# Kernel optimization log

Measured on AMD Instinct MI355X. Metric: run time of the kernel, lower is better.

## Reference

```python
import jax, jax.numpy as jnp
import numpy as np

N = 100000
NFEAT = 128
NHID = 128
NCLASS = 40
E = 1600000
EPS = 1e-5


def _spmm(vals, src, dst, x, n):
    # y[dst] += vals * x[src]  (sparse adj @ x)
    return jax.ops.segment_sum(vals[:, None] * x[src], dst, num_segments=n)


def _bn(h, gamma, beta, rmean, rvar):
    # BatchNorm1d in eval mode (running statistics)
    return (h - rmean) * jax.lax.rsqrt(rvar + EPS) * gamma + beta


def setup_inputs() -> dict:
    key = jax.random.key(0)
    ks = jax.random.split(key, 24)
    inp = {
        'x': jax.random.normal(ks[0], (N, NFEAT), dtype=jnp.float32),
        'M': jax.random.uniform(ks[1], (N, 1), dtype=jnp.float32),
        'AM': jax.random.uniform(ks[2], (N, 1), dtype=jnp.float32),
        'srcZ': jax.random.randint(ks[3], (E,), 0, N, dtype=jnp.int32),
        'dstZ': jax.random.randint(ks[4], (E,), 0, N, dtype=jnp.int32),
        'valsZ': jax.random.uniform(ks[5], (E,), dtype=jnp.float32),
        'src': jax.random.randint(ks[6], (E,), 0, N, dtype=jnp.int32),
        'dst': jax.random.randint(ks[7], (E,), 0, N, dtype=jnp.int32),
        'vals': jax.random.uniform(ks[8], (E,), dtype=jnp.float32),
        # layer 0 (PaGConv) params
        'W0': jax.random.normal(ks[9], (NHID, NFEAT), dtype=jnp.float32) * (1.414 / np.sqrt(NFEAT)),
        'b0': jnp.zeros((NHID,), dtype=jnp.float32),
        'g0': jnp.ones((NHID,), dtype=jnp.float32),
        'be0': jnp.zeros((NHID,), dtype=jnp.float32),
        'rm0': jax.random.normal(ks[10], (NHID,), dtype=jnp.float32) * 0.1,
        'rv0': jax.random.uniform(ks[11], (NHID,), dtype=jnp.float32) + 0.5,
        # layer 1 (GConv) params
        'W1': jax.random.normal(ks[12], (NHID, NHID), dtype=jnp.float32) * (1.414 / np.sqrt(NHID)),
        'b1': jnp.zeros((NHID,), dtype=jnp.float32),
        'g1': jnp.ones((NHID,), dtype=jnp.float32),
        'be1': jnp.zeros((NHID,), dtype=jnp.float32),
        'rm1': jax.random.normal(ks[13], (NHID,), dtype=jnp.float32) * 0.1,
        'rv1': jax.random.uniform(ks[14], (NHID,), dtype=jnp.float32) + 0.5,
        # layer 2 (GConv) params
        'W2': jax.random.normal(ks[15], (NCLASS, NHID), dtype=jnp.float32) * (1.414 / np.sqrt(NHID)),
        'b2': jnp.zeros((NCLASS,), dtype=jnp.float32),
    }
    return inp


def reference(x, M, AM, srcZ, dstZ, valsZ, src, dst, vals,
              W0, b0, g0, be0, rm0, rv0,
              W1, b1, g1, be1, rm1, rv1,
              W2, b2):
    n = x.shape[0]
    # layer 0: PaGConv with adjZ: fc(spmm(adjZ, M*x) * AM), then BN + ReLU (dropout off in eval)
    h = _spmm(valsZ, srcZ, dstZ, M * x, n) * AM
    h = h @ W0.T + b0
    h = jax.nn.relu(_bn(h, g0, be0, rm0, rv0))
    # layer 1: GConv with adj: fc(spmm(adj, h)), then BN + ReLU
    h = _spmm(vals, src, dst, h, n)
    h = h @ W1.T + b1
    h = jax.nn.relu(_bn(h, g1, be1, rm1, rv1))
    # layer 2: GConv, then log_softmax
    h = _spmm(vals, src, dst, h, n)
    h = h @ W2.T + b2
    return jax.nn.log_softmax(h, axis=-1)
```

## Files before the change

kernel.cpp:

```cpp
#include <hip/hip_runtime.h>
#include <math.h>

#define NFEAT 128
#define NCLS 40
#define NCLSP 64
#define BINROWS 64
#define NBINMAX 1600
#define NBLKC 256
#define CHUNKMAX 6400
#define SEGC 7
#define RSMAX 2048

typedef short bf16x8 __attribute__((ext_vector_type(8)));
typedef float f32x4 __attribute__((ext_vector_type(4)));

__device__ __forceinline__ float bf2f(unsigned int lo16) {
  return __uint_as_float((lo16 & 0xffffu) << 16);
}
__device__ __forceinline__ unsigned int f2bf(float x) {
  unsigned int u = __float_as_uint(x);
  return (u + 0x7fffu + ((u >> 16) & 1u)) >> 16;
}

__global__ void bn_prep(const float* b0, const float* g0, const float* be0,
                        const float* rm0, const float* rv0,
                        const float* b1, const float* g1, const float* be1,
                        const float* rm1, const float* rv1,
                        float* sc0, float* sh0, float* sc1, float* sh1) {
  int t = threadIdx.x;
  if (t < 128) {
    float s = g0[t] * rsqrtf(rv0[t] + 1e-5f);
    sc0[t] = s;
    sh0[t] = (b0[t] - rm0[t]) * s + be0[t];
  } else {
    int i = t - 128;
    float s = g1[i] * rsqrtf(rv1[i] + 1e-5f);
    sc1[i] = s;
    sh1[i] = (b1[i] - rm1[i]) * s + be1[i];
  }
}

__global__ void convert_xm(const float* __restrict__ x, const float* __restrict__ Mv,
                           unsigned short* __restrict__ xm, int n) {
  int i = blockIdx.x * 256 + threadIdx.x;
  if (i >= n * (NFEAT / 8)) return;
  int row = i >> 4;
  float m = Mv[row];
  const float4* p = (const float4*)(x + (size_t)i * 8);
  float4 v0 = p[0], v1 = p[1];
  unsigned int o0 = f2bf(v0.x * m) | (f2bf(v0.y * m) << 16);
  unsigned int o1 = f2bf(v0.z * m) | (f2bf(v0.w * m) << 16);
  unsigned int o2 = f2bf(v1.x * m) | (f2bf(v1.y * m) << 16);
  unsigned int o3 = f2bf(v1.z * m) | (f2bf(v1.w * m) << 16);
  ((uint4*)xm)[i] = make_uint4(o0, o1, o2, o3);
}

__global__ void convert_w(const float* __restrict__ W0, const float* __restrict__ W1,
                          const float* __restrict__ W2,
                          unsigned short* __restrict__ Wb0, unsigned short* __restrict__ Wb1,
                          unsigned short* __restrict__ W2hi, unsigned short* __restrict__ W2lo) {
  int i = blockIdx.x * 256 + threadIdx.x;
  if (i < 4096) {
    const float* W = (i < 2048) ? W0 : W1;
    unsigned short* Wb = (i < 2048) ? Wb0 : Wb1;
    int j = (i < 2048) ? i : i - 2048;
    const float4* p = (const float4*)(W + (size_t)j * 8);
    float4 v0 = p[0], v1 = p[1];
    unsigned int o0 = f2bf(v0.x) | (f2bf(v0.y) << 16);
    unsigned int o1 = f2bf(v0.z) | (f2bf(v0.w) << 16);
    unsigned int o2 = f2bf(v1.x) | (f2bf(v1.y) << 16);
    unsigned int o3 = f2bf(v1.z) | (f2bf(v1.w) << 16);
    ((uint4*)Wb)[j] = make_uint4(o0, o1, o2, o3);
  } else {
    int j = i - 4096;
    int r = j >> 4;
    float v[8] = {0.f, 0.f, 0.f, 0.f, 0.f, 0.f, 0.f, 0.f};
    if (r < NCLS) {
      const float4* p = (const float4*)(W2 + (size_t)j * 8);
      float4 a = p[0], b = p[1];
      v[0] = a.x; v[1] = a.y; v[2] = a.z; v[3] = a.w;
      v[4] = b.x; v[5] = b.y; v[6] = b.z; v[7] = b.w;
    }
    unsigned int h[8], l[8];
#pragma unroll
    for (int q = 0; q < 8; ++q) {
      h[q] = f2bf(v[q]);
      l[q] = f2bf(v[q] - bf2f(h[q]));
    }
    ((uint4*)W2hi)[j] = make_uint4(h[0] | (h[1] << 16), h[2] | (h[3] << 16),
                                   h[4] | (h[5] << 16), h[6] | (h[7] << 16));
    ((uint4*)W2lo)[j] = make_uint4(l[0] | (l[1] << 16), l[2] | (l[3] << 16),
                                   l[4] | (l[5] << 16), l[6] | (l[7] << 16));
  }
}

__global__ __launch_bounds__(256) void bin_sort1(
    const int* __restrict__ srcp, const int* __restrict__ dstp, const float* __restrict__ valp,
    int2* __restrict__ Drm, int2* __restrict__ binsC, int E, int nbin, int chunk) {
  __shared__ int2 stage[CHUNKMAX];
  __shared__ int cur[NBINMAX];
  __shared__ int ps[256];
  const int t = threadIdx.x, k = blockIdx.x;
  for (int i = t; i < nbin; i += 256) cur[i] = 0;
  __syncthreads();
  const int e0 = k * chunk, e1 = min(E, e0 + chunk);
#pragma unroll 4
  for (int e = e0 + t; e < e1; e += 256) atomicAdd(&cur[dstp[e] >> 6], 1);
  __syncthreads();
  int loc[SEGC], cnt[SEGC];
  int s = 0;
#pragma unroll
  for (int j = 0; j < SEGC; ++j) {
    int i = t * SEGC + j;
    int v = (i < nbin) ? cur[i] : 0;
    loc[j] = s; cnt[j] = v;
    s += v;
  }
  ps[t] = s;
  __syncthreads();
  for (int o = 1; o < 256; o <<= 1) {
    int x = (t >= o) ? ps[t - o] : 0;
    __syncthreads();
    ps[t] += x;
    __syncthreads();
  }
  int ex = ps[t] - s;
#pragma unroll
  for (int j = 0; j < SEGC; ++j) {
    int i = t * SEGC + j;
    if (i < nbin) {
      int o = ex + loc[j];
      Drm[(size_t)k * nbin + i] = make_int2(e0 + o, cnt[j]);
      cur[i] = o;
    }
  }
  __syncthreads();
#pragma unroll 2
  for (int e = e0 + t; e < e1; e += 256) {
    int d = dstp[e];
    int p = atomicAdd(&cur[d >> 6], 1);
    stage[p] = make_int2(srcp[e] | ((d & 63) << 17), __float_as_int(valp[e]));
  }
  __syncthreads();
  const int n = e1 - e0;
  for (int i = t; i < n; i += 256) binsC[e0 + i] = stage[i];
}

__global__ __launch_bounds__(256) void transposeD1(
    const int2* __restrict__ Drm, int2* __restrict__ Dbm, int* __restrict__ binTot, int nbin) {
  __shared__ int2 st[8][256];
  __shared__ int part[256];
  int t = threadIdx.x;
  int i0 = blockIdx.x * 8;
#pragma unroll
  for (int j = 0; j < 8; ++j) {
    int i = i0 + j;
    st[j][t] = (i < nbin) ? Drm[(size_t)t * nbin + i] : make_int2(0, 0);
  }
  __syncthreads();
  {
    int j = t >> 5, ks = (t & 31) * 8;
    int i = i0 + j;
    if (i < nbin) {
      int2* q = &Dbm[(size_t)i * NBLKC + ks];
#pragma unroll
      for (int m = 0; m < 8; ++m) q[m] = st[j][ks + m];
    }
    int p = 0;
#pragma unroll
    for (int m = 0; m < 8; ++m) p += st[j][ks + m].y;
    part[t] = p;
  }
  __syncthreads();
  if (t < 8) {
    int s = 0;
    for (int k = 0; k < 32; ++k) s += part[t * 32 + k];
    if (i0 + t < nbin) binTot[i0 + t] = s;
  }
}

__global__ __launch_bounds__(256) void bin_start1(
    const int* __restrict__ bt, int* __restrict__ bs, int nbin) {
  __shared__ int ps[256];
  int t = threadIdx.x;
  int C = (nbin + 255) / 256;
  int loc[SEGC + 1];
  int sum = 0;
  for (int j = 0; j < C; ++j) {
    int i = t * C + j;
    loc[j] = sum;
    sum += (i < nbin) ? bt[i] : 0;
  }
  ps[t] = sum;
  __syncthreads();
  for (int o = 1; o < 256; o <<= 1) {
    int x = (t >= o) ? ps[t - o] : 0;
    __syncthreads();
    ps[t] += x;
    __syncthreads();
  }
  int ex = ps[t] - sum;
  for (int j = 0; j < C; ++j) {
    int i = t * C + j;
    if (i < nbin) bs[i] = ex + loc[j];
  }
  if (t == 255) bs[nbin] = ps[255];
}

__global__ __launch_bounds__(256) void row_sort(
    const int2* __restrict__ Dbm, const int2* __restrict__ binsC,
    const int* __restrict__ binStart, int2* __restrict__ bins2,
    int* __restrict__ rowptr, int n, int nbin) {
  __shared__ int2 stage[RSMAX];
  __shared__ int ps[256];
  __shared__ int rcnt[BINROWS];
  __shared__ int roff[BINROWS];
  const int b = blockIdx.x, t = threadIdx.x;
  if (t < BINROWS) rcnt[t] = 0;
  int2 run = Dbm[(size_t)b * NBLKC + t];
  ps[t] = run.y;
  __syncthreads();
  for (int o = 1; o < 256; o <<= 1) {
    int x = (t >= o) ? ps[t - o] : 0;
    __syncthreads();
    ps[t] += x;
    __syncthreads();
  }
  int mystart = ps[t] - run.y;
  for (int j = 0; j < run.y; ++j) {
    int2 en = binsC[run.x + j];
    int idx = mystart + j;
    if (idx < RSMAX) stage[idx] = en;
    atomicAdd(&rcnt[(en.x >> 17) & 63], 1);
  }
  __syncthreads();
  const int bs = binStart[b];
  if (t < BINROWS) {
    int c = rcnt[t];
    int s = c;
#pragma unroll
    for (int o = 1; o < 64; o <<= 1) {
      int v = __shfl_up(s, o);
      if (t >= o) s += v;
    }
    int excl = s - c;
    int row = b * BINROWS + t;
    if (row < n) rowptr[row] = bs + excl;
    roff[t] = excl;
  }
  __syncthreads();
  int total = min(ps[255], RSMAX);
  for (int i = t; i < total; i += 256) {
    int2 en = stage[i];
    int row = (en.x >> 17) & 63;
    int p = atomicAdd(&roff[row], 1);
    bins2[bs + p] = en;
  }
  if (b == nbin - 1 && t == 0) rowptr[n] = binStart[nbin];
}

template <bool SCALE>
__global__ __launch_bounds__(256) void spmm128_sorted(
    const int* __restrict__ rowptr, const int2* __restrict__ bins2,
    const unsigned short* __restrict__ X, const float* __restrict__ AM,
    unsigned short* __restrict__ Y, int n) {
  int row = (blockIdx.x * 256 + threadIdx.x) >> 6;
  int lane = threadIdx.x & 63;
  if (row >= n) return;
  int s = rowptr[row], d = rowptr[row + 1] - s;
  int eidx = lane >> 4, l16 = lane & 15;
  float acc[8] = {0.f, 0.f, 0.f, 0.f, 0.f, 0.f, 0.f, 0.f};
  for (int kb = 0; kb < d; kb += 64) {
    int rem = min(64, d - kb);
    int2 my = (lane < rem) ? bins2[s + kb + lane] : make_int2(0, 0);
    int myc = my.x & 0x1FFFF;
    float myw = __int_as_float(my.y);
    int steps = (rem + 3) >> 2;
#pragma unroll 4
    for (int st = 0; st < steps; ++st) {
      int idx = st * 4 + eidx;
      int c = __shfl(myc, idx);
      float wv = __shfl(myw, idx);
      uint4 pv = *(const uint4*)(X + (size_t)c * NFEAT + l16 * 8);
      acc[0] += wv * bf2f(pv.x);
      acc[1] += wv * bf2f(pv.x >> 16);
      acc[2] += wv * bf2f(pv.y);
      acc[3] += wv * bf2f(pv.y >> 16);
      acc[4] += wv * bf2f(pv.z);
      acc[5] += wv * bf2f(pv.z >> 16);
      acc[6] += wv * bf2f(pv.w);
      acc[7] += wv * bf2f(pv.w >> 16);
    }
  }
#pragma unroll
  for (int j = 0; j < 8; ++j) {
    acc[j] += __shfl_xor(acc[j], 16);
    acc[j] += __shfl_xor(acc[j], 32);
  }
  if (SCALE) {
    float am = AM[row];
#pragma unroll
    for (int j = 0; j < 8; ++j) acc[j] *= am;
  }
  if (eidx == 0) {
    uint4 pk;
    pk.x = f2bf(acc[0]) | (f2bf(acc[1]) << 16);
    pk.y = f2bf(acc[2]) | (f2bf(acc[3]) << 16);
    pk.z = f2bf(acc[4]) | (f2bf(acc[5]) << 16);
    pk.w = f2bf(acc[6]) | (f2bf(acc[7]) << 16);
    *(uint4*)(Y + (size_t)row * NFEAT + l16 * 8) = pk;
  }
}

__global__ __launch_bounds__(256) void gemm_mfma128(
    const unsigned short* __restrict__ Y, const unsigned short* __restrict__ Wb,
    const float* __restrict__ scale, const float* __restrict__ shift,
    unsigned short* __restrict__ Out, int M) {
  const int wave = threadIdx.x >> 6;
  const int lane = threadIdx.x & 63;
  const int quad = lane >> 4;
  const int l16 = lane & 15;
  const int arow = blockIdx.x * 64 + wave * 16 + l16;
  const bool rv = arow < M;

  f32x4 acc[8];
#pragma unroll
  for (int c = 0; c < 8; ++c) acc[c] = (f32x4){0.f, 0.f, 0.f, 0.f};

#pragma unroll
  for (int kc = 0; kc < 128; kc += 32) {
    bf16x8 a = rv ? *(const bf16x8*)(Y + (size_t)arow * 128 + kc + quad * 8)
                  : (bf16x8){0, 0, 0, 0, 0, 0, 0, 0};
#pragma unroll
    for (int c = 0; c < 8; ++c) {
      bf16x8 b = *(const bf16x8*)(Wb + (size_t)(c * 16 + l16) * 128 + kc + quad * 8);
      acc[c] = __builtin_amdgcn_mfma_f32_16x16x32_bf16(a, b, acc[c], 0, 0, 0);
    }
  }

  int orow0 = blockIdx.x * 64 + wave * 16 + quad * 4;
#pragma unroll
  for (int c = 0; c < 8; ++c) {
    int col = c * 16 + l16;
    float sc = scale[col], sh = shift[col];
#pragma unroll
    for (int r = 0; r < 4; ++r) {
      int orow = orow0 + r;
      if (orow < M) {
        float v = fmaxf(acc[c][r] * sc + sh, 0.f);
        Out[(size_t)orow * 128 + col] = (unsigned short)f2bf(v);
      }
    }
  }
}

__global__ __launch_bounds__(256) void gemm40_mfma(
    const unsigned short* __restrict__ Y, const unsigned short* __restrict__ Whi,
    const unsigned short* __restrict__ Wlo, unsigned short* __restrict__ G2, int M) {
  const int wave = threadIdx.x >> 6;
  const int lane = threadIdx.x & 63;
  const int quad = lane >> 4;
  const int l16 = lane & 15;
  const int arow = blockIdx.x * 64 + wave * 16 + l16;
  const bool rv = arow < M;

  f32x4 acc[4];
#pragma unroll
  for (int c = 0; c < 4; ++c) acc[c] = (f32x4){0.f, 0.f, 0.f, 0.f};

#pragma unroll
  for (int kc = 0; kc < 128; kc += 32) {
    bf16x8 a = rv ? *(const bf16x8*)(Y + (size_t)arow * 128 + kc + quad * 8)
                  : (bf16x8){0, 0, 0, 0, 0, 0, 0, 0};
#pragma unroll
    for (int c = 0; c < 4; ++c) {
      bf16x8 bh = *(const bf16x8*)(Whi + (size_t)(c * 16 + l16) * 128 + kc + quad * 8);
      bf16x8 bl = *(const bf16x8*)(Wlo + (size_t)(c * 16 + l16) * 128 + kc + quad * 8);
      acc[c] = __builtin_amdgcn_mfma_f32_16x16x32_bf16(a, bh, acc[c], 0, 0, 0);
      acc[c] = __builtin_amdgcn_mfma_f32_16x16x32_bf16(a, bl, acc[c], 0, 0, 0);
    }
  }

  int orow0 = blockIdx.x * 64 + wave * 16 + quad * 4;
#pragma unroll
  for (int c = 0; c < 4; ++c) {
    int col = c * 16 + l16;
#pragma unroll
    for (int r = 0; r < 4; ++r) {
      int orow = orow0 + r;
      if (orow < M) G2[(size_t)orow * NCLSP + col] = (unsigned short)f2bf(acc[c][r]);
    }
  }
}

__global__ __launch_bounds__(256) void spmm_softmax64(
    const int* __restrict__ rowptr, const int2* __restrict__ bins2,
    const unsigned short* __restrict__ G2, const float* __restrict__ b2,
    float* __restrict__ out, int n) {
  int row = (blockIdx.x * 256 + threadIdx.x) >> 6;
  int lane = threadIdx.x & 63;
  if (row >= n) return;
  const int eidx = lane >> 3, oct = lane & 7;
  const bool vq = oct < (NCLS / 8);
  float4 bv0 = make_float4(0.f, 0.f, 0.f, 0.f), bv1 = bv0;
  if (vq) {
    bv0 = *(const float4*)(b2 + oct * 8);
    bv1 = *(const float4*)(b2 + oct * 8 + 4);
  }

  int s0i = rowptr[row], d = rowptr[row + 1] - s0i;
  float a[8] = {0.f, 0.f, 0.f, 0.f, 0.f, 0.f, 0.f, 0.f};
  for (int kb = 0; kb < d; kb += 64) {
    int rem = min(64, d - kb);
    int2 my = (lane < rem) ? bins2[s0i + kb + lane] : make_int2(0, 0);
    int myc = my.x & 0x1FFFF;
    float myw = __int_as_float(my.y);
    int steps = (rem + 7) >> 3;
#pragma unroll 2
    for (int st = 0; st < steps; ++st) {
      int idx = st * 8 + eidx;
      int c = __shfl(myc, idx);
      float wv = __shfl(myw, idx);
      uint4 pv = *(const uint4*)(G2 + (size_t)c * NCLSP + oct * 8);
      a[0] += wv * bf2f(pv.x);
      a[1] += wv * bf2f(pv.x >> 16);
      a[2] += wv * bf2f(pv.y);
      a[3] += wv * bf2f(pv.y >> 16);
      a[4] += wv * bf2f(pv.z);
      a[5] += wv * bf2f(pv.z >> 16);
      a[6] += wv * bf2f(pv.w);
      a[7] += wv * bf2f(pv.w >> 16);
    }
  }
#pragma unroll
  for (int j = 0; j < 8; ++j) {
    a[j] += __shfl_xor(a[j], 8);
    a[j] += __shfl_xor(a[j], 16);
    a[j] += __shfl_xor(a[j], 32);
  }
  float z[8];
  z[0] = a[0] + bv0.x; z[1] = a[1] + bv0.y; z[2] = a[2] + bv0.z; z[3] = a[3] + bv0.w;
  z[4] = a[4] + bv1.x; z[5] = a[5] + bv1.y; z[6] = a[6] + bv1.z; z[7] = a[7] + bv1.w;
  bool par = (eidx == 0) && vq;
  float m = -INFINITY;
  if (par) {
    m = fmaxf(fmaxf(fmaxf(z[0], z[1]), fmaxf(z[2], z[3])),
              fmaxf(fmaxf(z[4], z[5]), fmaxf(z[6], z[7])));
  }
#pragma unroll
  for (int o = 1; o < 64; o <<= 1) m = fmaxf(m, __shfl_xor(m, o));
  float ex = 0.f;
  if (par) {
#pragma unroll
    for (int j = 0; j < 8; ++j) ex += __expf(z[j] - m);
  }
#pragma unroll
  for (int o = 1; o < 64; o <<= 1) ex += __shfl_xor(ex, o);
  float lg = m + __logf(ex);
  if (par) {
    *(float4*)&out[(size_t)row * NCLS + oct * 8] =
        make_float4(z[0] - lg, z[1] - lg, z[2] - lg, z[3] - lg);
    *(float4*)&out[(size_t)row * NCLS + oct * 8 + 4] =
        make_float4(z[4] - lg, z[5] - lg, z[6] - lg, z[7] - lg);
  }
}


extern "C" void kernel_launch(void* const* d_in, const int* in_sizes, int n_in,
                              void* d_out, int out_size, void* d_ws, size_t ws_size,
                              hipStream_t stream) {
  const float* x    = (const float*)d_in[0];
  const float* Mv   = (const float*)d_in[1];
  const float* AM   = (const float*)d_in[2];
  const int* srcZ   = (const int*)d_in[3];
  const int* dstZ   = (const int*)d_in[4];
  const float* valsZ= (const float*)d_in[5];
  const int* src    = (const int*)d_in[6];
  const int* dst    = (const int*)d_in[7];
  const float* vals = (const float*)d_in[8];
  const float* W0   = (const float*)d_in[9];
  const float* b0   = (const float*)d_in[10];
  const float* g0   = (const float*)d_in[11];
  const float* be0  = (const float*)d_in[12];
  const float* rm0  = (const float*)d_in[13];
  const float* rv0  = (const float*)d_in[14];
  const float* W1   = (const float*)d_in[15];
  const float* b1   = (const float*)d_in[16];
  const float* g1   = (const float*)d_in[17];
  const float* be1  = (const float*)d_in[18];
  const float* rm1  = (const float*)d_in[19];
  const float* rv1  = (const float*)d_in[20];
  const float* W2   = (const float*)d_in[21];
  const float* b2   = (const float*)d_in[22];
  float* out = (float*)d_out;

  const int N = in_sizes[1];
  const int E = in_sizes[3];
  const int NBIN = (N + BINROWS - 1) / BINROWS;
  const int CHUNK = (E + NBLKC - 1) / NBLKC;

  char* w = (char*)d_ws;
  size_t off = 0;
  auto alloc = [&](size_t bytes) -> void* {
    void* p = w + off;
    off = (off + bytes + 255) & ~(size_t)255;
    return p;
  };
  int2* binsC = (int2*)alloc((size_t)NBLKC * CHUNK * 8);
  int2* Drm = (int2*)alloc((size_t)NBLKC * NBIN * 8);
  int2* Dbm = (int2*)alloc((size_t)NBIN * NBLKC * 8);
  int* binTot = (int*)alloc((size_t)NBIN * 4);
  int* binStart = (int*)alloc((size_t)(NBIN + 1) * 4);
  int2* bins2A = (int2*)alloc((size_t)E * 8);
  int* rowptrA = (int*)alloc((size_t)(N + 1) * 4);
  unsigned short* xm = (unsigned short*)alloc((size_t)N * NFEAT * 2);
  unsigned short* bufA = (unsigned short*)alloc((size_t)N * NFEAT * 2);
  unsigned short* bufB = (unsigned short*)alloc((size_t)N * NFEAT * 2);
  float* sc0 = (float*)alloc(128 * 4);
  float* sh0 = (float*)alloc(128 * 4);
  float* sc1 = (float*)alloc(128 * 4);
  float* sh1 = (float*)alloc(128 * 4);
  unsigned short* Wb0 = (unsigned short*)alloc(128 * 128 * 2);
  unsigned short* Wb1 = (unsigned short*)alloc(128 * 128 * 2);
  unsigned short* W2hi = (unsigned short*)alloc(64 * 128 * 2);
  unsigned short* W2lo = (unsigned short*)alloc(64 * 128 * 2);
  int2* bins2Z = (int2*)bufB;
  int* rowptrZ = (int*)((char*)bufB + 13 * 1024 * 1024);
  unsigned short* G2 = bufA;

  const int RB = (N + 3) / 4;
  const int GB64 = (N + 63) / 64;
  const int TDB = (NBIN + 7) / 8;

  bn_prep<<<1, 256, 0, stream>>>(b0, g0, be0, rm0, rv0, b1, g1, be1, rm1, rv1,
                                 sc0, sh0, sc1, sh1);
  convert_xm<<<(N * (NFEAT / 8) + 255) / 256, 256, 0, stream>>>(x, Mv, xm, N);
  convert_w<<<20, 256, 0, stream>>>(W0, W1, W2, Wb0, Wb1, W2hi, W2lo);

  bin_sort1<<<NBLKC, 256, 0, stream>>>(srcZ, dstZ, valsZ, Drm, binsC, E, NBIN, CHUNK);
  transposeD1<<<TDB, 256, 0, stream>>>(Drm, Dbm, binTot, NBIN);
  bin_start1<<<1, 256, 0, stream>>>(binTot, binStart, NBIN);
  row_sort<<<NBIN, 256, 0, stream>>>(Dbm, binsC, binStart, bins2Z, rowptrZ, N, NBIN);

  bin_sort1<<<NBLKC, 256, 0, stream>>>(src, dst, vals, Drm, binsC, E, NBIN, CHUNK);
  transposeD1<<<TDB, 256, 0, stream>>>(Drm, Dbm, binTot, NBIN);
  bin_start1<<<1, 256, 0, stream>>>(binTot, binStart, NBIN);
  row_sort<<<NBIN, 256, 0, stream>>>(Dbm, binsC, binStart, bins2A, rowptrA, N, NBIN);

  spmm128_sorted<true><<<RB, 256, 0, stream>>>(rowptrZ, bins2Z, xm, AM, bufA, N);
  gemm_mfma128<<<GB64, 256, 0, stream>>>(bufA, Wb0, sc0, sh0, bufB, N);

  spmm128_sorted<false><<<RB, 256, 0, stream>>>(rowptrA, bins2A, bufB,
                                                (const float*)nullptr, bufA, N);
  gemm_mfma128<<<GB64, 256, 0, stream>>>(bufA, Wb1, sc1, sh1, bufB, N);

  gemm40_mfma<<<GB64, 256, 0, stream>>>(bufB, W2hi, W2lo, G2, N);
  spmm_softmax64<<<RB, 256, 0, stream>>>(rowptrA, bins2A, G2, b2, out, N);
}
```

Before: 581.6 us.

## Batch both graph sorts into combined launches and retune SpMM lane mappings

Merges the BN-prep and weight-conversion kernels into one launch. The two adjacency sorting pipelines (bin sort, transpose, bin start, row sort) now each run as a single doubled-grid launch, which needs separate buffers, with the Drm/Dbm scratch placed in bufA. The 128-wide SpMM now has each half-wave take alternate edges with 4 features per lane and reads edges directly instead of through shuffles. The softmax SpMM switches to 4 classes per lane over 16 lanes. The aim is fewer launches, more parallelism in the small sort stages, and a different gather width trade-off, at the cost of narrower per-lane loads and extra workspace.

```diff
diff --git a/kernel.cpp b/kernel.cpp
--- a/kernel.cpp
+++ b/kernel.cpp
@@ -22,44 +22,31 @@
   return (u + 0x7fffu + ((u >> 16) & 1u)) >> 16;
 }
 
-__global__ void bn_prep(const float* b0, const float* g0, const float* be0,
-                        const float* rm0, const float* rv0,
-                        const float* b1, const float* g1, const float* be1,
-                        const float* rm1, const float* rv1,
-                        float* sc0, float* sh0, float* sc1, float* sh1) {
+__global__ __launch_bounds__(256) void prep_misc(
+    const float* b0, const float* g0, const float* be0,
+    const float* rm0, const float* rv0,
+    const float* b1, const float* g1, const float* be1,
+    const float* rm1, const float* rv1,
+    float* sc0, float* sh0, float* sc1, float* sh1,
+    const float* __restrict__ W0, const float* __restrict__ W1,
+    const float* __restrict__ W2,
+    unsigned short* __restrict__ Wb0, unsigned short* __restrict__ Wb1,
+    unsigned short* __restrict__ W2hi, unsigned short* __restrict__ W2lo) {
   int t = threadIdx.x;
-  if (t < 128) {
-    float s = g0[t] * rsqrtf(rv0[t] + 1e-5f);
-    sc0[t] = s;
-    sh0[t] = (b0[t] - rm0[t]) * s + be0[t];
-  } else {
-    int i = t - 128;
-    float s = g1[i] * rsqrtf(rv1[i] + 1e-5f);
-    sc1[i] = s;
-    sh1[i] = (b1[i] - rm1[i]) * s + be1[i];
-  }
-}
-
-__global__ void convert_xm(const float* __restrict__ x, const float* __restrict__ Mv,
-                           unsigned short* __restrict__ xm, int n) {
-  int i = blockIdx.x * 256 + threadIdx.x;
-  if (i >= n * (NFEAT / 8)) return;
-  int row = i >> 4;
-  float m = Mv[row];
-  const float4* p = (const float4*)(x + (size_t)i * 8);
-  float4 v0 = p[0], v1 = p[1];
-  unsigned int o0 = f2bf(v0.x * m) | (f2bf(v0.y * m) << 16);
-  unsigned int o1 = f2bf(v0.z * m) | (f2bf(v0.w * m) << 16);
-  unsigned int o2 = f2bf(v1.x * m) | (f2bf(v1.y * m) << 16);
-  unsigned int o3 = f2bf(v1.z * m) | (f2bf(v1.w * m) << 16);
-  ((uint4*)xm)[i] = make_uint4(o0, o1, o2, o3);
-}
-
-__global__ void convert_w(const float* __restrict__ W0, const float* __restrict__ W1,
-                          const float* __restrict__ W2,
-                          unsigned short* __restrict__ Wb0, unsigned short* __restrict__ Wb1,
-                          unsigned short* __restrict__ W2hi, unsigned short* __restrict__ W2lo) {
-  int i = blockIdx.x * 256 + threadIdx.x;
+  if (blockIdx.x == 0) {
+    if (t < 128) {
+      float s = g0[t] * rsqrtf(rv0[t] + 1e-5f);
+      sc0[t] = s;
+      sh0[t] = (b0[t] - rm0[t]) * s + be0[t];
+    } else {
+      int i = t - 128;
+      float s = g1[i] * rsqrtf(rv1[i] + 1e-5f);
+      sc1[i] = s;
+      sh1[i] = (b1[i] - rm1[i]) * s + be1[i];
+    }
+    return;
+  }
+  int i = (blockIdx.x - 1) * 256 + t;
   if (i < 4096) {
     const float* W = (i < 2048) ? W0 : W1;
     unsigned short* Wb = (i < 2048) ? Wb0 : Wb1;
@@ -94,13 +81,39 @@
   }
 }
 
-__global__ __launch_bounds__(256) void bin_sort1(
-    const int* __restrict__ srcp, const int* __restrict__ dstp, const float* __restrict__ valp,
-    int2* __restrict__ Drm, int2* __restrict__ binsC, int E, int nbin, int chunk) {
+__global__ void convert_xm(const float* __restrict__ x, const float* __restrict__ Mv,
+                           unsigned short* __restrict__ xm, int n) {
+  int i = blockIdx.x * 256 + threadIdx.x;
+  if (i >= n * (NFEAT / 8)) return;
+  int row = i >> 4;
+  float m = Mv[row];
+  const float4* p = (const float4*)(x + (size_t)i * 8);
+  float4 v0 = p[0], v1 = p[1];
+  unsigned int o0 = f2bf(v0.x * m) | (f2bf(v0.y * m) << 16);
+  unsigned int o1 = f2bf(v0.z * m) | (f2bf(v0.w * m) << 16);
+  unsigned int o2 = f2bf(v1.x * m) | (f2bf(v1.y * m) << 16);
+  unsigned int o3 = f2bf(v1.z * m) | (f2bf(v1.w * m) << 16);
+  ((uint4*)xm)[i] = make_uint4(o0, o1, o2, o3);
+}
+
+__global__ __launch_bounds__(256) void bin_sort2(
+    const int* __restrict__ srcZ, const int* __restrict__ dstZ, const float* __restrict__ valZ,
+    const int* __restrict__ srcA, const int* __restrict__ dstA, const float* __restrict__ valA,
+    int2* __restrict__ DrmZ, int2* __restrict__ DrmA,
+    int2* __restrict__ binsCZ, int2* __restrict__ binsCA,
+    int E, int nbin, int chunk) {
   __shared__ int2 stage[CHUNKMAX];
   __shared__ int cur[NBINMAX];
   __shared__ int ps[256];
-  const int t = threadIdx.x, k = blockIdx.x;
+  const int t = threadIdx.x;
+  int k = blockIdx.x;
+  const int* srcp; const int* dstp; const float* valp; int2* Drm; int2* binsC;
+  if (k < NBLKC) {
+    srcp = srcZ; dstp = dstZ; valp = valZ; Drm = DrmZ; binsC = binsCZ;
+  } else {
+    k -= NBLKC;
+    srcp = srcA; dstp = dstA; valp = valA; Drm = DrmA; binsC = binsCA;
+  }
   for (int i = t; i < nbin; i += 256) cur[i] = 0;
   __syncthreads();
   const int e0 = k * chunk, e1 = min(E, e0 + chunk);
@@ -146,12 +159,22 @@
   for (int i = t; i < n; i += 256) binsC[e0 + i] = stage[i];
 }
 
-__global__ __launch_bounds__(256) void transposeD1(
-    const int2* __restrict__ Drm, int2* __restrict__ Dbm, int* __restrict__ binTot, int nbin) {
+__global__ __launch_bounds__(256) void transposeD2(
+    const int2* __restrict__ DrmZ, const int2* __restrict__ DrmA,
+    int2* __restrict__ DbmZ, int2* __restrict__ DbmA,
+    int* __restrict__ binTotZ, int* __restrict__ binTotA, int nbin, int tdb) {
   __shared__ int2 st[8][256];
   __shared__ int part[256];
   int t = threadIdx.x;
-  int i0 = blockIdx.x * 8;
+  int b = blockIdx.x;
+  const int2* Drm; int2* Dbm; int* binTot;
+  if (b < tdb) {
+    Drm = DrmZ; Dbm = DbmZ; binTot = binTotZ;
+  } else {
+    b -= tdb;
+    Drm = DrmA; Dbm = DbmA; binTot = binTotA;
+  }
+  int i0 = b * 8;
 #pragma unroll
   for (int j = 0; j < 8; ++j) {
     int i = i0 + j;
@@ -179,10 +202,13 @@
   }
 }
 
-__global__ __launch_bounds__(256) void bin_start1(
-    const int* __restrict__ bt, int* __restrict__ bs, int nbin) {
+__global__ __launch_bounds__(256) void bin_start2(
+    const int* __restrict__ btZ, const int* __restrict__ btA,
+    int* __restrict__ bsZ, int* __restrict__ bsA, int nbin) {
   __shared__ int ps[256];
   int t = threadIdx.x;
+  const int* bt = (blockIdx.x == 0) ? btZ : btA;
+  int* bs = (blockIdx.x == 0) ? bsZ : bsA;
   int C = (nbin + 255) / 256;
   int loc[SEGC + 1];
   int sum = 0;
@@ -207,15 +233,25 @@
   if (t == 255) bs[nbin] = ps[255];
 }
 
-__global__ __launch_bounds__(256) void row_sort(
-    const int2* __restrict__ Dbm, const int2* __restrict__ binsC,
-    const int* __restrict__ binStart, int2* __restrict__ bins2,
-    int* __restrict__ rowptr, int n, int nbin) {
+__global__ __launch_bounds__(256) void row_sort2(
+    const int2* __restrict__ DbmZ, const int2* __restrict__ DbmA,
+    const int2* __restrict__ binsCZ, const int2* __restrict__ binsCA,
+    const int* __restrict__ binStartZ, const int* __restrict__ binStartA,
+    int2* __restrict__ bins2Z, int2* __restrict__ bins2A,
+    int* __restrict__ rowptrZ, int* __restrict__ rowptrA, int n, int nbin) {
   __shared__ int2 stage[RSMAX];
   __shared__ int ps[256];
   __shared__ int rcnt[BINROWS];
   __shared__ int roff[BINROWS];
-  const int b = blockIdx.x, t = threadIdx.x;
+  int b = blockIdx.x;
+  const int t = threadIdx.x;
+  const int2* Dbm; const int2* binsC; const int* binStart; int2* bins2; int* rowptr;
+  if (b < nbin) {
+    Dbm = DbmZ; binsC = binsCZ; binStart = binStartZ; bins2 = bins2Z; rowptr = rowptrZ;
+  } else {
+    b -= nbin;
+    Dbm = DbmA; binsC = binsCA; binStart = binStartA; bins2 = bins2A; rowptr = rowptrA;
+  }
   if (t < BINROWS) rcnt[t] = 0;
   int2 run = Dbm[(size_t)b * NBLKC + t];
   ps[t] = run.y;
@@ -267,49 +303,45 @@
   int row = (blockIdx.x * 256 + threadIdx.x) >> 6;
   int lane = threadIdx.x & 63;
   if (row >= n) return;
-  int s = rowptr[row], d = rowptr[row + 1] - s;
-  int eidx = lane >> 4, l16 = lane & 15;
-  float acc[8] = {0.f, 0.f, 0.f, 0.f, 0.f, 0.f, 0.f, 0.f};
-  for (int kb = 0; kb < d; kb += 64) {
-    int rem = min(64, d - kb);
-    int2 my = (lane < rem) ? bins2[s + kb + lane] : make_int2(0, 0);
-    int myc = my.x & 0x1FFFF;
-    float myw = __int_as_float(my.y);
-    int steps = (rem + 3) >> 2;
-#pragma unroll 4
-    for (int st = 0; st < steps; ++st) {
-      int idx = st * 4 + eidx;
-      int c = __shfl(myc, idx);
-      float wv = __shfl(myw, idx);
-      uint4 pv = *(const uint4*)(X + (size_t)c * NFEAT + l16 * 8);
-      acc[0] += wv * bf2f(pv.x);
-      acc[1] += wv * bf2f(pv.x >> 16);
-      acc[2] += wv * bf2f(pv.y);
-      acc[3] += wv * bf2f(pv.y >> 16);
-      acc[4] += wv * bf2f(pv.z);
-      acc[5] += wv * bf2f(pv.z >> 16);
-      acc[6] += wv * bf2f(pv.w);
-      acc[7] += wv * bf2f(pv.w >> 16);
-    }
-  }
-#pragma unroll
-  for (int j = 0; j < 8; ++j) {
-    acc[j] += __shfl_xor(acc[j], 16);
-    acc[j] += __shfl_xor(acc[j], 32);
-  }
+  int s = rowptr[row], dend = rowptr[row + 1];
+  int half = lane >> 5, l32 = lane & 31;
+  float s0 = 0.f, s1 = 0.f, s2 = 0.f, s3 = 0.f;
+  int e = s;
+  for (; e + 8 <= dend; e += 8) {
+#pragma unroll
+    for (int st = 0; st < 4; ++st) {
+      int2 en = bins2[e + 2 * st + half];
+      int c = en.x & 0x1FFFF;
+      float wv = __int_as_float(en.y);
+      uint2 pv = *(const uint2*)(X + (size_t)c * NFEAT + l32 * 4);
+      s0 += wv * bf2f(pv.x);
+      s1 += wv * bf2f(pv.x >> 16);
+      s2 += wv * bf2f(pv.y);
+      s3 += wv * bf2f(pv.y >> 16);
+    }
+  }
+  if (e < dend) {
+#pragma unroll
+    for (int st = 0; st < 4; ++st) {
+      int ee = e + 2 * st + half;
+      int2 en = (ee < dend) ? bins2[ee] : make_int2(0, 0);
+      int c = en.x & 0x1FFFF;
+      float wv = __int_as_float(en.y);
+      uint2 pv = *(const uint2*)(X + (size_t)c * NFEAT + l32 * 4);
+      s0 += wv * bf2f(pv.x);
+      s1 += wv * bf2f(pv.x >> 16);
+      s2 += wv * bf2f(pv.y);
+      s3 += wv * bf2f(pv.y >> 16);
+    }
+  }
+  s0 += __shfl_xor(s0, 32); s1 += __shfl_xor(s1, 32);
+  s2 += __shfl_xor(s2, 32); s3 += __shfl_xor(s3, 32);
   if (SCALE) {
     float am = AM[row];
-#pragma unroll
-    for (int j = 0; j < 8; ++j) acc[j] *= am;
-  }
-  if (eidx == 0) {
-    uint4 pk;
-    pk.x = f2bf(acc[0]) | (f2bf(acc[1]) << 16);
-    pk.y = f2bf(acc[2]) | (f2bf(acc[3]) << 16);
-    pk.z = f2bf(acc[4]) | (f2bf(acc[5]) << 16);
-    pk.w = f2bf(acc[6]) | (f2bf(acc[7]) << 16);
-    *(uint4*)(Y + (size_t)row * NFEAT + l16 * 8) = pk;
-  }
+    s0 *= am; s1 *= am; s2 *= am; s3 *= am;
+  }
+  unsigned int pk = half ? (f2bf(s2) | (f2bf(s3) << 16)) : (f2bf(s0) | (f2bf(s1) << 16));
+  ((unsigned int*)Y)[(size_t)row * (NFEAT / 2) + l32 * 2 + half] = pk;
 }
 
 __global__ __launch_bounds__(256) void gemm_mfma128(
@@ -400,68 +432,46 @@
   int row = (blockIdx.x * 256 + threadIdx.x) >> 6;
   int lane = threadIdx.x & 63;
   if (row >= n) return;
-  const int eidx = lane >> 3, oct = lane & 7;
-  const bool vq = oct < (NCLS / 8);
-  float4 bv0 = make_float4(0.f, 0.f, 0.f, 0.f), bv1 = bv0;
-  if (vq) {
-    bv0 = *(const float4*)(b2 + oct * 8);
-    bv1 = *(const float4*)(b2 + oct * 8 + 4);
-  }
+  const int eidx = lane >> 4, q = lane & 15;
+  const bool vq = q < (NCLS / 4);
+  float4 bv = vq ? *(const float4*)(b2 + q * 4) : make_float4(0.f, 0.f, 0.f, 0.f);
 
   int s0i = rowptr[row], d = rowptr[row + 1] - s0i;
-  float a[8] = {0.f, 0.f, 0.f, 0.f, 0.f, 0.f, 0.f, 0.f};
+  float a0 = 0.f, a1 = 0.f, a2 = 0.f, a3 = 0.f;
   for (int kb = 0; kb < d; kb += 64) {
     int rem = min(64, d - kb);
     int2 my = (lane < rem) ? bins2[s0i + kb + lane] : make_int2(0, 0);
     int myc = my.x & 0x1FFFF;
     float myw = __int_as_float(my.y);
-    int steps = (rem + 7) >> 3;
-#pragma unroll 2
+    int steps = (rem + 3) >> 2;
+#pragma unroll 4
     for (int st = 0; st < steps; ++st) {
-      int idx = st * 8 + eidx;
+      int idx = st * 4 + eidx;
       int c = __shfl(myc, idx);
       float wv = __shfl(myw, idx);
-      uint4 pv = *(const uint4*)(G2 + (size_t)c * NCLSP + oct * 8);
-      a[0] += wv * bf2f(pv.x);
-      a[1] += wv * bf2f(pv.x >> 16);
-      a[2] += wv * bf2f(pv.y);
-      a[3] += wv * bf2f(pv.y >> 16);
-      a[4] += wv * bf2f(pv.z);
-      a[5] += wv * bf2f(pv.z >> 16);
-      a[6] += wv * bf2f(pv.w);
-      a[7] += wv * bf2f(pv.w >> 16);
-    }
-  }
-#pragma unroll
-  for (int j = 0; j < 8; ++j) {
-    a[j] += __shfl_xor(a[j], 8);
-    a[j] += __shfl_xor(a[j], 16);
-    a[j] += __shfl_xor(a[j], 32);
-  }
-  float z[8];
-  z[0] = a[0] + bv0.x; z[1] = a[1] + bv0.y; z[2] = a[2] + bv0.z; z[3] = a[3] + bv0.w;
-  z[4] = a[4] + bv1.x; z[5] = a[5] + bv1.y; z[6] = a[6] + bv1.z; z[7] = a[7] + bv1.w;
+      uint2 pv = *(const uint2*)(G2 + (size_t)c * NCLSP + q * 4);
+      a0 += wv * bf2f(pv.x);
+      a1 += wv * bf2f(pv.x >> 16);
+      a2 += wv * bf2f(pv.y);
+      a3 += wv * bf2f(pv.y >> 16);
+    }
+  }
+  a0 += __shfl_xor(a0, 16); a1 += __shfl_xor(a1, 16);
+  a2 += __shfl_xor(a2, 16); a3 += __shfl_xor(a3, 16);
+  a0 += __shfl_xor(a0, 32); a1 += __shfl_xor(a1, 32);
+  a2 += __shfl_xor(a2, 32); a3 += __shfl_xor(a3, 32);
+  float z0 = a0 + bv.x, z1 = a1 + bv.y, z2 = a2 + bv.z, z3 = a3 + bv.w;
   bool par = (eidx == 0) && vq;
-  float m = -INFINITY;
-  if (par) {
-    m = fmaxf(fmaxf(fmaxf(z[0], z[1]), fmaxf(z[2], z[3])),
-              fmaxf(fmaxf(z[4], z[5]), fmaxf(z[6], z[7])));
-  }
+  float m = par ? fmaxf(fmaxf(z0, z1), fmaxf(z2, z3)) : -INFINITY;
 #pragma unroll
   for (int o = 1; o < 64; o <<= 1) m = fmaxf(m, __shfl_xor(m, o));
-  float ex = 0.f;
-  if (par) {
-#pragma unroll
-    for (int j = 0; j < 8; ++j) ex += __expf(z[j] - m);
-  }
+  float ex = par ? (__expf(z0 - m) + __expf(z1 - m) + __expf(z2 - m) + __expf(z3 - m)) : 0.f;
 #pragma unroll
   for (int o = 1; o < 64; o <<= 1) ex += __shfl_xor(ex, o);
   float lg = m + __logf(ex);
   if (par) {
-    *(float4*)&out[(size_t)row * NCLS + oct * 8] =
-        make_float4(z[0] - lg, z[1] - lg, z[2] - lg, z[3] - lg);
-    *(float4*)&out[(size_t)row * NCLS + oct * 8 + 4] =
-        make_float4(z[4] - lg, z[5] - lg, z[6] - lg, z[7] - lg);
+    *(float4*)&out[(size_t)row * NCLS + q * 4] =
+        make_float4(z0 - lg, z1 - lg, z2 - lg, z3 - lg);
   }
 }
 
@@ -506,11 +516,12 @@
     off = (off + bytes + 255) & ~(size_t)255;
     return p;
   };
-  int2* binsC = (int2*)alloc((size_t)NBLKC * CHUNK * 8);
-  int2* Drm = (int2*)alloc((size_t)NBLKC * NBIN * 8);
-  int2* Dbm = (int2*)alloc((size_t)NBIN * NBLKC * 8);
-  int* binTot = (int*)alloc((size_t)NBIN * 4);
-  int* binStart = (int*)alloc((size_t)(NBIN + 1) * 4);
+  int2* binsCZ = (int2*)alloc((size_t)NBLKC * CHUNK * 8);
+  int2* binsCA = (int2*)alloc((size_t)NBLKC * CHUNK * 8);
+  int* binTotZ = (int*)alloc((size_t)NBIN * 4);
+  int* binTotA = (int*)alloc((size_t)NBIN * 4);
+  int* binStartZ = (int*)alloc((size_t)(NBIN + 1) * 4);
+  int* binStartA = (int*)alloc((size_t)(NBIN + 1) * 4);
   int2* bins2A = (int2*)alloc((size_t)E * 8);
   int* rowptrA = (int*)alloc((size_t)(N + 1) * 4);
   unsigned short* xm = (unsigned short*)alloc((size_t)N * NFEAT * 2);
@@ -524,6 +535,11 @@
   unsigned short* Wb1 = (unsigned short*)alloc(128 * 128 * 2);
   unsigned short* W2hi = (unsigned short*)alloc(64 * 128 * 2);
   unsigned short* W2lo = (unsigned short*)alloc(64 * 128 * 2);
+  const size_t drmBytes = (size_t)NBLKC * NBIN * 8;
+  int2* DrmZ = (int2*)((char*)bufA + 0 * drmBytes);
+  int2* DrmA = (int2*)((char*)bufA + 1 * drmBytes);
+  int2* DbmZ = (int2*)((char*)bufA + 2 * drmBytes);
+  int2* DbmA = (int2*)((char*)bufA + 3 * drmBytes);
   int2* bins2Z = (int2*)bufB;
   int* rowptrZ = (int*)((char*)bufB + 13 * 1024 * 1024);
   unsigned short* G2 = bufA;
@@ -532,20 +548,18 @@
   const int GB64 = (N + 63) / 64;
   const int TDB = (NBIN + 7) / 8;
 
-  bn_prep<<<1, 256, 0, stream>>>(b0, g0, be0, rm0, rv0, b1, g1, be1, rm1, rv1,
-                                 sc0, sh0, sc1, sh1);
+  prep_misc<<<21, 256, 0, stream>>>(b0, g0, be0, rm0, rv0, b1, g1, be1, rm1, rv1,
+                                    sc0, sh0, sc1, sh1, W0, W1, W2,
+                                    Wb0, Wb1, W2hi, W2lo);
   convert_xm<<<(N * (NFEAT / 8) + 255) / 256, 256, 0, stream>>>(x, Mv, xm, N);
-  convert_w<<<20, 256, 0, stream>>>(W0, W1, W2, Wb0, Wb1, W2hi, W2lo);
-
-  bin_sort1<<<NBLKC, 256, 0, stream>>>(srcZ, dstZ, valsZ, Drm, binsC, E, NBIN, CHUNK);
-  transposeD1<<<TDB, 256, 0, stream>>>(Drm, Dbm, binTot, NBIN);
-  bin_start1<<<1, 256, 0, stream>>>(binTot, binStart, NBIN);
-  row_sort<<<NBIN, 256, 0, stream>>>(Dbm, binsC, binStart, bins2Z, rowptrZ, N, NBIN);
-
-  bin_sort1<<<NBLKC, 256, 0, stream>>>(src, dst, vals, Drm, binsC, E, NBIN, CHUNK);
-  transposeD1<<<TDB, 256, 0, stream>>>(Drm, Dbm, binTot, NBIN);
-  bin_start1<<<1, 256, 0, stream>>>(binTot, binStart, NBIN);
-  row_sort<<<NBIN, 256, 0, stream>>>(Dbm, binsC, binStart, bins2A, rowptrA, N, NBIN);
+
+  bin_sort2<<<2 * NBLKC, 256, 0, stream>>>(srcZ, dstZ, valsZ, src, dst, vals,
+                                           DrmZ, DrmA, binsCZ, binsCA, E, NBIN, CHUNK);
+  transposeD2<<<2 * TDB, 256, 0, stream>>>(DrmZ, DrmA, DbmZ, DbmA, binTotZ, binTotA,
+                                           NBIN, TDB);
+  bin_start2<<<2, 256, 0, stream>>>(binTotZ, binTotA, binStartZ, binStartA, NBIN);
+  row_sort2<<<2 * NBIN, 256, 0, stream>>>(DbmZ, DbmA, binsCZ, binsCA, binStartZ, binStartA,
+                                          bins2Z, bins2A, rowptrZ, rowptrA, N, NBIN);
 
   spmm128_sorted<true><<<RB, 256, 0, stream>>>(rowptrZ, bins2Z, xm, AM, bufA, N);
   gemm_mfma128<<<GB64, 256, 0, stream>>>(bufA, Wb0, sc0, sh0, bufB, N);
```

Result: faster. 546.4 us (-6.0%).
